# Optimization experiments

Measured on AMD Instinct MI355X. Metric: run time of the kernel, lower is better.

The kernel has to match this reference:

```python
import jax, jax.numpy as jnp
import numpy as np

N, E, G = 10000, 40000, 128          # nodes, edges, graphs
NF, EF, H, NH, GD, L = 92, 50, 64, 10, 108, 5  # feat dims, hidden, heads, global dim, layers
EPS = 1e-5

def _lrelu(v):
    return jax.nn.leaky_relu(v, 0.2)

def setup_inputs() -> dict:
    key = jax.random.key(0)
    ks = jax.random.split(key, 24)
    def rn(k, shp, s=0.05):
        return jax.random.normal(k, shp, jnp.float32) * s
    return {
        "x": jax.random.normal(ks[0], (N, NF), jnp.float32),
        "edge_index": jax.random.randint(ks[1], (2, E), 0, N, dtype=jnp.int32),
        "edge_attr": jax.random.normal(ks[2], (E, EF), jnp.float32),
        "batch_idx": jnp.sort(jax.random.randint(ks[3], (N,), 0, G, dtype=jnp.int32)),
        "global_features": jax.random.normal(ks[4], (G, GD), jnp.float32),
        "node_W": rn(ks[5], (NF, H)), "node_b": jnp.zeros((H,), jnp.float32),
        "edge_W": rn(ks[6], (EF, H)), "edge_b": jnp.zeros((H,), jnp.float32),
        "conv_W": rn(ks[7], (L, 2 * H, NH * H)),
        "conv_att": rn(ks[8], (L, NH, 2 * H)),
        "conv_b": jnp.zeros((L, H), jnp.float32),
        "conv_gamma": jnp.ones((L, NH), jnp.float32),
        "conv_beta": jnp.zeros((L, NH), jnp.float32),
        "ga_W1": rn(ks[9], (H + GD, H)), "ga_b1": jnp.zeros((H,), jnp.float32),
        "ga_W2": rn(ks[10], (H, 1)), "ga_b2": jnp.zeros((1,), jnp.float32),
        "out_W1": rn(ks[11], (H, H)), "out_b1": jnp.zeros((H,), jnp.float32),
        "out_W2": rn(ks[12], (H, 1)), "out_b2": jnp.zeros((1,), jnp.float32),
    }

def reference(x, edge_index, edge_attr, batch_idx, global_features,
              node_W, node_b, edge_W, edge_b,
              conv_W, conv_att, conv_b, conv_gamma, conv_beta,
              ga_W1, ga_b1, ga_W2, ga_b2, out_W1, out_b1, out_W2, out_b2):
    row, col = edge_index[0], edge_index[1]
    # embeddings
    h = _lrelu(x @ node_W + node_b)            # [N, H]
    ea = _lrelu(edge_attr @ edge_W + edge_b)   # [E, H]
    initial = h
    inv_std = 1.0 / jnp.sqrt(1.0 + EPS)        # DiffGroupNorm eval: running mean=0, var=1
    for i in range(L):
        xi = jnp.concatenate([h[row], ea], axis=-1)               # [E, 2H]
        xj = jnp.concatenate([h[col], ea], axis=-1)
        hi = _lrelu(xi @ conv_W[i]).reshape(E, NH, H)             # [E, NH, H]
        hj = _lrelu(xj @ conv_W[i]).reshape(E, NH, H)
        alpha = jnp.sum(jnp.concatenate([hi, hj], -1) * conv_att[i][None], -1)  # [E, NH]
        alpha = _lrelu(alpha)
        alpha = alpha * inv_std * conv_gamma[i] + conv_beta[i]
        alpha = jax.nn.softmax(alpha, axis=1)                     # softmax over heads
        msg = (hj * alpha[..., None]).reshape(E, NH * H)
        agg = jax.ops.segment_sum(msg, row, num_segments=N).reshape(N, NH, H)
        h_new = agg.mean(axis=1) + conv_b[i]
        h = h + h_new if i > 0 else h_new
    h = h + initial
    # global attention: softmax over nodes within each graph
    g = global_features[batch_idx]                                 # [N, GD]
    s = _lrelu(jnp.concatenate([h, g], -1) @ ga_W1 + ga_b1)
    score = (s @ ga_W2 + ga_b2)[:, 0]                              # [N]
    smax = jax.ops.segment_max(score, batch_idx, num_segments=G)
    ex = jnp.exp(score - smax[batch_idx])
    denom = jax.ops.segment_sum(ex, batch_idx, num_segments=G)
    w = (ex / denom[batch_idx])[:, None]
    h = h * w
    pooled = jax.ops.segment_sum(h, batch_idx, num_segments=G)     # [G, H]
    out = jax.nn.relu(pooled @ out_W1 + out_b1) @ out_W2 + out_b2
    return out[:, 0]
```

## Files before the change

### kernel.cpp

```cpp
#include <hip/hip_runtime.h>

#define LRELU(v) ((v) > 0.f ? (v) : 0.2f * (v))

template <int CTRL, int RMASK>
__device__ __forceinline__ float dpp_add(float v) {
  int moved = __builtin_amdgcn_update_dpp(0, __builtin_bit_cast(int, v), CTRL,
                                          RMASK, 0xf, true);
  return v + __builtin_bit_cast(float, moved);
}
__device__ __forceinline__ float wave_sum(float v) {
  v = dpp_add<0x111, 0xf>(v);
  v = dpp_add<0x112, 0xf>(v);
  v = dpp_add<0x114, 0xf>(v);
  v = dpp_add<0x118, 0xf>(v);
  v = dpp_add<0x142, 0xa>(v);
  v = dpp_add<0x143, 0xc>(v);
  return __builtin_bit_cast(
      float, __builtin_amdgcn_readlane(__builtin_bit_cast(int, v), 63));
}

__global__ __launch_bounds__(256) void embed2_kernel(
    const float* __restrict__ x, const float* __restrict__ nW,
    const float* __restrict__ nb, float* __restrict__ h0, int N_,
    const float* __restrict__ eattr, const float* __restrict__ eW,
    const float* __restrict__ eb, float* __restrict__ ea, int E_,
    int nodeBlocks) {
  const int lane = threadIdx.x & 63;
  const float *X, *W, *b;
  float* out;
  int M, K, r;
  if ((int)blockIdx.x < nodeBlocks) {
    r = blockIdx.x * 4 + (threadIdx.x >> 6);
    X = x; W = nW; b = nb; out = h0; M = N_; K = 92;
  } else {
    r = (blockIdx.x - nodeBlocks) * 4 + (threadIdx.x >> 6);
    X = eattr; W = eW; b = eb; out = ea; M = E_; K = 50;
  }
  r = __builtin_amdgcn_readfirstlane(r);
  if (r >= M) return;
  float acc = b[lane];
  const float* Xr = X + (size_t)r * K;
  const float* Wl = W + lane;
  for (int k = 0; k < K; ++k) acc = fmaf(Xr[k], Wl[(size_t)k * 64], acc);
  acc = LRELU(acc);
  out[(size_t)r * 64 + lane] = acc;
}

__global__ __launch_bounds__(256, 4) void update_gemm_kernel(
    const float* __restrict__ A0, float* __restrict__ h,
    float* __restrict__ agg, const float* __restrict__ bvec,
    const float* __restrict__ W, float* __restrict__ P, int M, int mode) {
  const int lane = threadIdx.x & 63;
  const int wv =
      __builtin_amdgcn_readfirstlane(blockIdx.x * 4 + (threadIdx.x >> 6));
  const int r0 = wv * 4;
  if (r0 >= M) return;
  float hv[4];
  if (mode < 0) {
#pragma unroll
    for (int r = 0; r < 4; ++r) hv[r] = A0[(size_t)(r0 + r) * 64 + lane];
  } else {
    float bl = bvec[lane];
#pragma unroll
    for (int r = 0; r < 4; ++r) {
      size_t idx = (size_t)(r0 + r) * 64 + lane;
      float v = fmaf(agg[idx], 0.1f, bl);
      if (mode >= 1) v += h[idx];
      agg[idx] = 0.f;
      h[idx] = v;
      hv[r] = v;
    }
  }
  float acc[4][10];
#pragma unroll
  for (int r = 0; r < 4; ++r)
#pragma unroll
    for (int q = 0; q < 10; ++q) acc[r][q] = 0.f;
  const float* Wl = W + lane;
  float wa[10], wb[10];
#pragma unroll
  for (int q = 0; q < 10; ++q) wa[q] = Wl[q * 64];
#pragma unroll 1
  for (int k = 0; k < 64; k += 2) {
#pragma unroll
    for (int q = 0; q < 10; ++q) wb[q] = Wl[(k + 1) * 640 + q * 64];
#pragma unroll
    for (int r = 0; r < 4; ++r) {
      float a = __shfl(hv[r], k);
#pragma unroll
      for (int q = 0; q < 10; ++q) acc[r][q] = fmaf(a, wa[q], acc[r][q]);
    }
    if (k + 2 < 64) {
#pragma unroll
      for (int q = 0; q < 10; ++q) wa[q] = Wl[(k + 2) * 640 + q * 64];
    }
#pragma unroll
    for (int r = 0; r < 4; ++r) {
      float a = __shfl(hv[r], k + 1);
#pragma unroll
      for (int q = 0; q < 10; ++q) acc[r][q] = fmaf(a, wb[q], acc[r][q]);
    }
  }
#pragma unroll
  for (int r = 0; r < 4; ++r) {
    float* Crow = P + (size_t)(r0 + r) * 640;
#pragma unroll
    for (int q = 0; q < 10; ++q) Crow[q * 64 + lane] = acc[r][q];
  }
}

__global__ __launch_bounds__(256, 3) void edge_fused_kernel(
    const float* __restrict__ P, const float* __restrict__ ea,
    const float* __restrict__ Wbot,
    const int* __restrict__ row, const int* __restrict__ col,
    const float* __restrict__ att, const float* __restrict__ gamma,
    const float* __restrict__ beta, float* __restrict__ agg, int E_) {
  const int lane = threadIdx.x & 63;
  const int wv =
      __builtin_amdgcn_readfirstlane(blockIdx.x * 4 + (threadIdx.x >> 6));
  const int e0 = wv * 8;
  if (e0 >= E_) return;

  int eix[8], ris[8], cis[8];
#pragma unroll
  for (int r = 0; r < 8; ++r) {
    int e = (e0 + r < E_) ? (e0 + r) : (E_ - 1);
    eix[r] = e;
    ris[r] = row[e];
    cis[r] = col[e];
  }

  float qacc[8][10];
#pragma unroll
  for (int r = 0; r < 8; ++r)
#pragma unroll
    for (int q = 0; q < 10; ++q) qacc[r][q] = 0.f;

  const float* Wl = Wbot + lane;
  float wa[10], wb[10];
#pragma unroll
  for (int q = 0; q < 10; ++q) wa[q] = Wl[q * 64];
#pragma unroll 1
  for (int k = 0; k < 64; k += 2) {
#pragma unroll
    for (int q = 0; q < 10; ++q) wb[q] = Wl[(k + 1) * 640 + q * 64];
#pragma unroll
    for (int r = 0; r < 8; ++r) {
      float a = ea[(size_t)eix[r] * 64 + k];
#pragma unroll
      for (int q = 0; q < 10; ++q) qacc[r][q] = fmaf(a, wa[q], qacc[r][q]);
    }
    if (k + 2 < 64) {
#pragma unroll
      for (int q = 0; q < 10; ++q) wa[q] = Wl[(k + 2) * 640 + q * 64];
    }
#pragma unroll
    for (int r = 0; r < 8; ++r) {
      float a = ea[(size_t)eix[r] * 64 + k + 1];
#pragma unroll
      for (int q = 0; q < 10; ++q) qacc[r][q] = fmaf(a, wb[q], qacc[r][q]);
    }
  }

  const float inv_std = 0.9999950000374997f;
  float gm[10], bt[10];
#pragma unroll
  for (int q = 0; q < 10; ++q) {
    gm[q] = gamma[q];
    bt[q] = beta[q];
  }

  float prb[10], pcb[10];
  {
    const float* Pr = P + (size_t)ris[0] * 640 + lane;
    const float* Pc = P + (size_t)cis[0] * 640 + lane;
#pragma unroll
    for (int q = 0; q < 10; ++q) {
      prb[q] = Pr[q * 64];
      pcb[q] = Pc[q * 64];
    }
  }

#pragma unroll
  for (int r = 0; r < 8; ++r) {
    if (e0 + r >= E_) break;
    float pr[10], pc[10];
#pragma unroll
    for (int q = 0; q < 10; ++q) {
      pr[q] = prb[q];
      pc[q] = pcb[q];
    }
    if (r + 1 < 8) {
      const float* Pr = P + (size_t)ris[r + 1] * 640 + lane;
      const float* Pc = P + (size_t)cis[r + 1] * 640 + lane;
#pragma unroll
      for (int q = 0; q < 10; ++q) {
        prb[q] = Pr[q * 64];
        pcb[q] = Pc[q * 64];
      }
    }
    float hj[10], sv[10];
#pragma unroll
    for (int q = 0; q < 10; ++q) {
      float qc = qacc[r][q];
      float hi = pr[q] + qc;
      float hjv = pc[q] + qc;
      hi = LRELU(hi);
      hjv = LRELU(hjv);
      hj[q] = hjv;
      float part =
          fmaf(hi, att[q * 128 + lane], hjv * att[q * 128 + 64 + lane]);
      sv[q] = wave_sum(part);
    }
    float mx = -1e30f;
#pragma unroll
    for (int q = 0; q < 10; ++q) {
      float a = sv[q];
      a = LRELU(a);
      a = fmaf(a * inv_std, gm[q], bt[q]);
      sv[q] = a;
      mx = fmaxf(mx, a);
    }
    float ssum = 0.f;
#pragma unroll
    for (int q = 0; q < 10; ++q) {
      float ex = __expf(sv[q] - mx);
      sv[q] = ex;
      ssum += ex;
    }
    float inv = 1.0f / ssum;
    float m = 0.f;
#pragma unroll
    for (int q = 0; q < 10; ++q) m = fmaf(sv[q] * inv, hj[q], m);
    atomicAdd(agg + (size_t)ris[r] * 64 + lane, m);
  }
}

__global__ __launch_bounds__(256) void finalize_kernel(
    float* __restrict__ h, float* __restrict__ agg, const float* __restrict__ b,
    const float* __restrict__ h0, int total) {
  int idx = blockIdx.x * 256 + threadIdx.x;
  if (idx >= total) return;
  int f = idx & 63;
  float v = fmaf(agg[idx], 0.1f, b[f]);
  agg[idx] = 0.f;
  h[idx] = v + h[idx] + h0[idx];
}

__global__ __launch_bounds__(256) void score_kernel(
    const float* __restrict__ h, const int* __restrict__ batch,
    const float* __restrict__ gf, const float* __restrict__ W1,
    const float* __restrict__ b1, const float* __restrict__ W2,
    const float* __restrict__ b2, float* __restrict__ score, int N_) {
  const int lane = threadIdx.x & 63;
  const int n =
      __builtin_amdgcn_readfirstlane(blockIdx.x * 4 + (threadIdx.x >> 6));
  if (n >= N_) return;
  float acc = b1[lane];
  const float* hn = h + (size_t)n * 64;
  const float* W1l = W1 + lane;
#pragma unroll 8
  for (int k = 0; k < 64; ++k) acc = fmaf(hn[k], W1l[k * 64], acc);
  const int bn = batch[n];
  const float* g = gf + (size_t)bn * 108;
#pragma unroll 4
  for (int k = 0; k < 108; ++k) acc = fmaf(g[k], W1l[(64 + k) * 64], acc);
  acc = LRELU(acc);
  float v = wave_sum(acc * W2[lane]);
  if (lane == 0) score[n] = v + b2[0];
}

__global__ void bounds_kernel(const int* __restrict__ batch,
                              int* __restrict__ start, int N_, int G_) {
  int n = blockIdx.x * blockDim.x + threadIdx.x;
  if (n >= N_) return;
  int b = batch[n];
  int bp = (n == 0) ? -1 : batch[n - 1];
  for (int g = bp + 1; g <= b; ++g) start[g] = n;
  if (n == N_ - 1)
    for (int g = b + 1; g <= G_; ++g) start[g] = N_;
}

__global__ __launch_bounds__(256) void pool_out_kernel(
    const float* __restrict__ h, const float* __restrict__ score,
    const int* __restrict__ start, const float* __restrict__ W1,
    const float* __restrict__ b1, const float* __restrict__ W2,
    const float* __restrict__ b2, float* __restrict__ out) {
  int g = blockIdx.x;
  int s0 = start[g], s1 = start[g + 1];
  int tid = threadIdx.x;
  __shared__ float red[256];
  __shared__ float pool[64];
  __shared__ float sh_smax, sh_denom;
  float lm = -1e30f;
  for (int n = s0 + tid; n < s1; n += 256) lm = fmaxf(lm, score[n]);
  red[tid] = lm;
  __syncthreads();
  for (int off = 128; off; off >>= 1) {
    if (tid < off) red[tid] = fmaxf(red[tid], red[tid + off]);
    __syncthreads();
  }
  if (tid == 0) sh_smax = red[0];
  __syncthreads();
  float smax = sh_smax;
  __syncthreads();
  float ls = 0.f;
  for (int n = s0 + tid; n < s1; n += 256) ls += __expf(score[n] - smax);
  red[tid] = ls;
  __syncthreads();
  for (int off = 128; off; off >>= 1) {
    if (tid < off) red[tid] += red[tid + off];
    __syncthreads();
  }
  if (tid == 0) sh_denom = red[0];
  __syncthreads();
  float denom = sh_denom;
  float invd = denom > 0.f ? 1.0f / denom : 0.f;
  __syncthreads();
  int f = tid & 63, sub = tid >> 6;
  float acc = 0.f;
  for (int n = s0 + sub; n < s1; n += 4)
    acc = fmaf(__expf(score[n] - smax), h[(size_t)n * 64 + f], acc);
  red[tid] = acc;
  __syncthreads();
  if (tid < 64)
    pool[tid] =
        (red[tid] + red[tid + 64] + red[tid + 128] + red[tid + 192]) * invd;
  __syncthreads();
  if (tid < 64) {
    float a = b1[tid];
#pragma unroll 8
    for (int k = 0; k < 64; ++k) a = fmaf(pool[k], W1[k * 64 + tid], a);
    a = fmaxf(a, 0.f);
    red[tid] = a * W2[tid];
  }
  __syncthreads();
  if (tid == 0) {
    float s = 0.f;
    for (int k = 0; k < 64; ++k) s += red[k];
    out[g] = s + b2[0];
  }
}

extern "C" void kernel_launch(void* const* d_in, const int* in_sizes, int n_in,
                              void* d_out, int out_size, void* d_ws,
                              size_t ws_size, hipStream_t stream) {
  const float* x          = (const float*)d_in[0];
  const int*   edge_index = (const int*)d_in[1];
  const float* edge_attr  = (const float*)d_in[2];
  const int*   batch_idx  = (const int*)d_in[3];
  const float* gf         = (const float*)d_in[4];
  const float* node_W     = (const float*)d_in[5];
  const float* node_b     = (const float*)d_in[6];
  const float* edge_W     = (const float*)d_in[7];
  const float* edge_b     = (const float*)d_in[8];
  const float* conv_W     = (const float*)d_in[9];
  const float* conv_att   = (const float*)d_in[10];
  const float* conv_b     = (const float*)d_in[11];
  const float* conv_gamma = (const float*)d_in[12];
  const float* conv_beta  = (const float*)d_in[13];
  const float* ga_W1      = (const float*)d_in[14];
  const float* ga_b1      = (const float*)d_in[15];
  const float* ga_W2      = (const float*)d_in[16];
  const float* ga_b2      = (const float*)d_in[17];
  const float* out_W1     = (const float*)d_in[18];
  const float* out_b1     = (const float*)d_in[19];
  const float* out_W2     = (const float*)d_in[20];
  const float* out_b2     = (const float*)d_in[21];
  float* out = (float*)d_out;

  const int N = in_sizes[3];
  const int E = in_sizes[2] / 50;
  const int G = in_sizes[4] / 108;
  const int L = 5;

  float* ws = (float*)d_ws;
  float* h    = ws;  ws += (size_t)N * 64;
  float* h0   = ws;  ws += (size_t)N * 64;
  float* ea   = ws;  ws += (size_t)E * 64;
  float* P    = ws;  ws += (size_t)N * 640;
  float* agg  = ws;  ws += (size_t)N * 64;
  float* scr  = ws;  ws += N;
  int* gstart = (int*)ws;

  const int* row = edge_index;
  const int* col = edge_index + E;

  int nodeBlocks = (N + 3) / 4;
  int edgeBlocks = (E + 3) / 4;
  embed2_kernel<<<nodeBlocks + edgeBlocks, 256, 0, stream>>>(
      x, node_W, node_b, h0, N, edge_attr, edge_W, edge_b, ea, E, nodeBlocks);
  (void)hipMemsetAsync(agg, 0, (size_t)N * 64 * sizeof(float), stream);

  for (int i = 0; i < L; ++i) {
    const float* Wi = conv_W + (size_t)i * 128 * 640;
    if (i == 0) {
      update_gemm_kernel<<<(N / 4 + 3) / 4, 256, 0, stream>>>(
          h0, h, agg, nullptr, Wi, P, N, -1);
    } else {
      update_gemm_kernel<<<(N / 4 + 3) / 4, 256, 0, stream>>>(
          nullptr, h, agg, conv_b + (i - 1) * 64, Wi, P, N,
          (i - 1) == 0 ? 0 : 1);
    }
    int waves = (E + 7) / 8;
    edge_fused_kernel<<<(waves + 3) / 4, 256, 0, stream>>>(
        P, ea, Wi + 64 * 640, row, col, conv_att + (size_t)i * 1280,
        conv_gamma + i * 10, conv_beta + i * 10, agg, E);
  }
  finalize_kernel<<<(N * 64 + 255) / 256, 256, 0, stream>>>(
      h, agg, conv_b + (L - 1) * 64, h0, N * 64);

  score_kernel<<<(N + 3) / 4, 256, 0, stream>>>(h, batch_idx, gf, ga_W1, ga_b1,
                                                ga_W2, ga_b2, scr, N);
  bounds_kernel<<<(N + 255) / 256, 256, 0, stream>>>(batch_idx, gstart, N, G);
  pool_out_kernel<<<G, 256, 0, stream>>>(h, scr, gstart, out_W1, out_b1, out_W2,
                                         out_b2, out);
}
```

Before: 688.6 us.

## Split edge kernel heads into two chunks with online softmax to cut registers

```diff
diff --git a/kernel.cpp b/kernel.cpp
--- a/kernel.cpp
+++ b/kernel.cpp
@@ -109,7 +109,7 @@
   }
 }
 
-__global__ __launch_bounds__(256, 3) void edge_fused_kernel(
+__global__ __launch_bounds__(256, 4) void edge_fused_kernel(
     const float* __restrict__ P, const float* __restrict__ ea,
     const float* __restrict__ Wbot,
     const int* __restrict__ row, const int* __restrict__ col,
@@ -130,109 +130,131 @@
     cis[r] = col[e];
   }
 
-  float qacc[8][10];
-#pragma unroll
-  for (int r = 0; r < 8; ++r)
-#pragma unroll
-    for (int q = 0; q < 10; ++q) qacc[r][q] = 0.f;
-
-  const float* Wl = Wbot + lane;
-  float wa[10], wb[10];
-#pragma unroll
-  for (int q = 0; q < 10; ++q) wa[q] = Wl[q * 64];
+  const float inv_std = 0.9999950000374997f;
+  float m[8];
+  float mx[8], ss[8];
+#pragma unroll
+  for (int r = 0; r < 8; ++r) {
+    m[r] = 0.f;
+    mx[r] = -1e30f;
+    ss[r] = 0.f;
+  }
+
 #pragma unroll 1
-  for (int k = 0; k < 64; k += 2) {
-#pragma unroll
-    for (int q = 0; q < 10; ++q) wb[q] = Wl[(k + 1) * 640 + q * 64];
+  for (int c = 0; c < 2; ++c) {
+    float qacc[8][5];
+#pragma unroll
+    for (int r = 0; r < 8; ++r)
+#pragma unroll
+      for (int q = 0; q < 5; ++q) qacc[r][q] = 0.f;
+    const float* Wl = Wbot + c * 320 + lane;
+    float wa[5], wb[5];
+#pragma unroll
+    for (int q = 0; q < 5; ++q) wa[q] = Wl[q * 64];
+#pragma unroll 1
+    for (int k = 0; k < 64; k += 2) {
+#pragma unroll
+      for (int q = 0; q < 5; ++q) wb[q] = Wl[(k + 1) * 640 + q * 64];
+#pragma unroll
+      for (int r = 0; r < 8; ++r) {
+        float a = ea[(size_t)eix[r] * 64 + k];
+#pragma unroll
+        for (int q = 0; q < 5; ++q) qacc[r][q] = fmaf(a, wa[q], qacc[r][q]);
+      }
+      if (k + 2 < 64) {
+#pragma unroll
+        for (int q = 0; q < 5; ++q) wa[q] = Wl[(k + 2) * 640 + q * 64];
+      }
+#pragma unroll
+      for (int r = 0; r < 8; ++r) {
+        float a = ea[(size_t)eix[r] * 64 + k + 1];
+#pragma unroll
+        for (int q = 0; q < 5; ++q) qacc[r][q] = fmaf(a, wb[q], qacc[r][q]);
+      }
+    }
+
+    float at_i[5], at_j[5];
+    float gm[5], bt[5];
+#pragma unroll
+    for (int q = 0; q < 5; ++q) {
+      at_i[q] = att[(c * 5 + q) * 128 + lane];
+      at_j[q] = att[(c * 5 + q) * 128 + 64 + lane];
+      gm[q] = gamma[c * 5 + q];
+      bt[q] = beta[c * 5 + q];
+    }
+
+    float prb[5], pcb[5];
+    {
+      const float* Pr = P + (size_t)ris[0] * 640 + c * 320 + lane;
+      const float* Pc = P + (size_t)cis[0] * 640 + c * 320 + lane;
+#pragma unroll
+      for (int q = 0; q < 5; ++q) {
+        prb[q] = Pr[q * 64];
+        pcb[q] = Pc[q * 64];
+      }
+    }
+
 #pragma unroll
     for (int r = 0; r < 8; ++r) {
-      float a = ea[(size_t)eix[r] * 64 + k];
-#pragma unroll
-      for (int q = 0; q < 10; ++q) qacc[r][q] = fmaf(a, wa[q], qacc[r][q]);
-    }
-    if (k + 2 < 64) {
-#pragma unroll
-      for (int q = 0; q < 10; ++q) wa[q] = Wl[(k + 2) * 640 + q * 64];
-    }
-#pragma unroll
-    for (int r = 0; r < 8; ++r) {
-      float a = ea[(size_t)eix[r] * 64 + k + 1];
-#pragma unroll
-      for (int q = 0; q < 10; ++q) qacc[r][q] = fmaf(a, wb[q], qacc[r][q]);
-    }
-  }
-
-  const float inv_std = 0.9999950000374997f;
-  float gm[10], bt[10];
-#pragma unroll
-  for (int q = 0; q < 10; ++q) {
-    gm[q] = gamma[q];
-    bt[q] = beta[q];
-  }
-
-  float prb[10], pcb[10];
-  {
-    const float* Pr = P + (size_t)ris[0] * 640 + lane;
-    const float* Pc = P + (size_t)cis[0] * 640 + lane;
-#pragma unroll
-    for (int q = 0; q < 10; ++q) {
-      prb[q] = Pr[q * 64];
-      pcb[q] = Pc[q * 64];
+      if (e0 + r >= E_) break;
+      float pr[5], pc[5];
+#pragma unroll
+      for (int q = 0; q < 5; ++q) {
+        pr[q] = prb[q];
+        pc[q] = pcb[q];
+      }
+      if (r + 1 < 8) {
+        const float* Pr = P + (size_t)ris[r + 1] * 640 + c * 320 + lane;
+        const float* Pc = P + (size_t)cis[r + 1] * 640 + c * 320 + lane;
+#pragma unroll
+        for (int q = 0; q < 5; ++q) {
+          prb[q] = Pr[q * 64];
+          pcb[q] = Pc[q * 64];
+        }
+      }
+      float hj[5], sv[5];
+#pragma unroll
+      for (int q = 0; q < 5; ++q) {
+        float qc = qacc[r][q];
+        float hi = pr[q] + qc;
+        float hjv = pc[q] + qc;
+        hi = LRELU(hi);
+        hjv = LRELU(hjv);
+        hj[q] = hjv;
+        float part = fmaf(hi, at_i[q], hjv * at_j[q]);
+        sv[q] = wave_sum(part);
+      }
+      float mxc = -1e30f;
+#pragma unroll
+      for (int q = 0; q < 5; ++q) {
+        float a = sv[q];
+        a = LRELU(a);
+        a = fmaf(a * inv_std, gm[q], bt[q]);
+        sv[q] = a;
+        mxc = fmaxf(mxc, a);
+      }
+      float nm = fmaxf(mx[r], mxc);
+      float scale = __expf(mx[r] - nm);
+      float sum5 = 0.f;
+#pragma unroll
+      for (int q = 0; q < 5; ++q) {
+        float ex = __expf(sv[q] - nm);
+        sv[q] = ex;
+        sum5 += ex;
+      }
+      ss[r] = fmaf(ss[r], scale, sum5);
+      float add = 0.f;
+#pragma unroll
+      for (int q = 0; q < 5; ++q) add = fmaf(sv[q], hj[q], add);
+      m[r] = fmaf(m[r], scale, add);
+      mx[r] = nm;
     }
   }
 
 #pragma unroll
   for (int r = 0; r < 8; ++r) {
     if (e0 + r >= E_) break;
-    float pr[10], pc[10];
-#pragma unroll
-    for (int q = 0; q < 10; ++q) {
-      pr[q] = prb[q];
-      pc[q] = pcb[q];
-    }
-    if (r + 1 < 8) {
-      const float* Pr = P + (size_t)ris[r + 1] * 640 + lane;
-      const float* Pc = P + (size_t)cis[r + 1] * 640 + lane;
-#pragma unroll
-      for (int q = 0; q < 10; ++q) {
-        prb[q] = Pr[q * 64];
-        pcb[q] = Pc[q * 64];
-      }
-    }
-    float hj[10], sv[10];
-#pragma unroll
-    for (int q = 0; q < 10; ++q) {
-      float qc = qacc[r][q];
-      float hi = pr[q] + qc;
-      float hjv = pc[q] + qc;
-      hi = LRELU(hi);
-      hjv = LRELU(hjv);
-      hj[q] = hjv;
-      float part =
-          fmaf(hi, att[q * 128 + lane], hjv * att[q * 128 + 64 + lane]);
-      sv[q] = wave_sum(part);
-    }
-    float mx = -1e30f;
-#pragma unroll
-    for (int q = 0; q < 10; ++q) {
-      float a = sv[q];
-      a = LRELU(a);
-      a = fmaf(a * inv_std, gm[q], bt[q]);
-      sv[q] = a;
-      mx = fmaxf(mx, a);
-    }
-    float ssum = 0.f;
-#pragma unroll
-    for (int q = 0; q < 10; ++q) {
-      float ex = __expf(sv[q] - mx);
-      sv[q] = ex;
-      ssum += ex;
-    }
-    float inv = 1.0f / ssum;
-    float m = 0.f;
-#pragma unroll
-    for (int q = 0; q < 10; ++q) m = fmaf(sv[q] * inv, hj[q], m);
-    atomicAdd(agg + (size_t)ris[r] * 64 + lane, m);
+    atomicAdd(agg + (size_t)ris[r] * 64 + lane, m[r] / ss[r]);
   }
 }
 
```

Measured after the change: 792.1 us. 15.0% more time.

## Fuse finalize into score kernel, binary-search graph bounds, raise edge occupancy

Applied to the files above, without the earlier changes.

```diff
diff --git a/kernel.cpp b/kernel.cpp
--- a/kernel.cpp
+++ b/kernel.cpp
@@ -109,7 +109,7 @@
   }
 }
 
-__global__ __launch_bounds__(256, 3) void edge_fused_kernel(
+__global__ __launch_bounds__(256, 4) void edge_fused_kernel(
     const float* __restrict__ P, const float* __restrict__ ea,
     const float* __restrict__ Wbot,
     const int* __restrict__ row, const int* __restrict__ col,
@@ -236,31 +236,24 @@
   }
 }
 
-__global__ __launch_bounds__(256) void finalize_kernel(
-    float* __restrict__ h, float* __restrict__ agg, const float* __restrict__ b,
-    const float* __restrict__ h0, int total) {
-  int idx = blockIdx.x * 256 + threadIdx.x;
-  if (idx >= total) return;
-  int f = idx & 63;
-  float v = fmaf(agg[idx], 0.1f, b[f]);
-  agg[idx] = 0.f;
-  h[idx] = v + h[idx] + h0[idx];
-}
-
-__global__ __launch_bounds__(256) void score_kernel(
-    const float* __restrict__ h, const int* __restrict__ batch,
-    const float* __restrict__ gf, const float* __restrict__ W1,
-    const float* __restrict__ b1, const float* __restrict__ W2,
-    const float* __restrict__ b2, float* __restrict__ score, int N_) {
+__global__ __launch_bounds__(256) void score_finalize_kernel(
+    float* __restrict__ h, const float* __restrict__ agg,
+    const float* __restrict__ cb, const float* __restrict__ h0,
+    const int* __restrict__ batch, const float* __restrict__ gf,
+    const float* __restrict__ W1, const float* __restrict__ b1,
+    const float* __restrict__ W2, const float* __restrict__ b2,
+    float* __restrict__ score, int N_) {
   const int lane = threadIdx.x & 63;
   const int n =
       __builtin_amdgcn_readfirstlane(blockIdx.x * 4 + (threadIdx.x >> 6));
   if (n >= N_) return;
+  size_t idx = (size_t)n * 64 + lane;
+  float hv = h[idx] + fmaf(agg[idx], 0.1f, cb[lane]) + h0[idx];
+  h[idx] = hv;
   float acc = b1[lane];
-  const float* hn = h + (size_t)n * 64;
   const float* W1l = W1 + lane;
 #pragma unroll 8
-  for (int k = 0; k < 64; ++k) acc = fmaf(hn[k], W1l[k * 64], acc);
+  for (int k = 0; k < 64; ++k) acc = fmaf(__shfl(hv, k), W1l[k * 64], acc);
   const int bn = batch[n];
   const float* g = gf + (size_t)bn * 108;
 #pragma unroll 4
@@ -270,28 +263,34 @@
   if (lane == 0) score[n] = v + b2[0];
 }
 
-__global__ void bounds_kernel(const int* __restrict__ batch,
-                              int* __restrict__ start, int N_, int G_) {
-  int n = blockIdx.x * blockDim.x + threadIdx.x;
-  if (n >= N_) return;
-  int b = batch[n];
-  int bp = (n == 0) ? -1 : batch[n - 1];
-  for (int g = bp + 1; g <= b; ++g) start[g] = n;
-  if (n == N_ - 1)
-    for (int g = b + 1; g <= G_; ++g) start[g] = N_;
-}
-
 __global__ __launch_bounds__(256) void pool_out_kernel(
     const float* __restrict__ h, const float* __restrict__ score,
-    const int* __restrict__ start, const float* __restrict__ W1,
+    const int* __restrict__ batch, int N_, const float* __restrict__ W1,
     const float* __restrict__ b1, const float* __restrict__ W2,
     const float* __restrict__ b2, float* __restrict__ out) {
   int g = blockIdx.x;
-  int s0 = start[g], s1 = start[g + 1];
   int tid = threadIdx.x;
+  __shared__ int sh_s0, sh_s1;
   __shared__ float red[256];
   __shared__ float pool[64];
   __shared__ float sh_smax, sh_denom;
+  if (tid == 0) {
+    int lo = 0, hi = N_;
+    while (lo < hi) {
+      int mid = (lo + hi) >> 1;
+      if (batch[mid] < g) lo = mid + 1; else hi = mid;
+    }
+    sh_s0 = lo;
+  } else if (tid == 1) {
+    int lo = 0, hi = N_;
+    while (lo < hi) {
+      int mid = (lo + hi) >> 1;
+      if (batch[mid] < g + 1) lo = mid + 1; else hi = mid;
+    }
+    sh_s1 = lo;
+  }
+  __syncthreads();
+  int s0 = sh_s0, s1 = sh_s1;
   float lm = -1e30f;
   for (int n = s0 + tid; n < s1; n += 256) lm = fmaxf(lm, score[n]);
   red[tid] = lm;
@@ -381,7 +380,6 @@
   float* P    = ws;  ws += (size_t)N * 640;
   float* agg  = ws;  ws += (size_t)N * 64;
   float* scr  = ws;  ws += N;
-  int* gstart = (int*)ws;
 
   const int* row = edge_index;
   const int* col = edge_index + E;
@@ -407,12 +405,10 @@
         P, ea, Wi + 64 * 640, row, col, conv_att + (size_t)i * 1280,
         conv_gamma + i * 10, conv_beta + i * 10, agg, E);
   }
-  finalize_kernel<<<(N * 64 + 255) / 256, 256, 0, stream>>>(
-      h, agg, conv_b + (L - 1) * 64, h0, N * 64);
-
-  score_kernel<<<(N + 3) / 4, 256, 0, stream>>>(h, batch_idx, gf, ga_W1, ga_b1,
-                                                ga_W2, ga_b2, scr, N);
-  bounds_kernel<<<(N + 255) / 256, 256, 0, stream>>>(batch_idx, gstart, N, G);
-  pool_out_kernel<<<G, 256, 0, stream>>>(h, scr, gstart, out_W1, out_b1, out_W2,
-                                         out_b2, out);
-}
+
+  score_finalize_kernel<<<(N + 3) / 4, 256, 0, stream>>>(
+      h, agg, conv_b + (L - 1) * 64, h0, batch_idx, gf, ga_W1, ga_b1, ga_W2,
+      ga_b2, scr, N);
+  pool_out_kernel<<<G, 256, 0, stream>>>(h, scr, batch_idx, N, out_W1, out_b1,
+                                         out_W2, out_b2, out);
+}
```

Measured after the change: 683.5 us. Within noise of the previous version (-0.7%).
